# Kernel optimization log

Hardware: AMD Instinct MI355X
Metric: run time of the kernel (lower is better)

## Reference

```python
import jax, jax.numpy as jnp
import numpy as np


def setup_inputs() -> dict:
    key = jax.random.key(0)
    k1, k2 = jax.random.split(key)
    B, H, W, D, K = 32, 32, 32, 256, 8192
    x = jax.random.normal(k1, (B, H, W, D), dtype=jnp.float32)
    # tf.random_uniform_initializer default: U(-0.05, 0.05), shape (embedding_dim, n_embeddings)
    embeddings = jax.random.uniform(k2, (D, K), dtype=jnp.float32, minval=-0.05, maxval=0.05)
    return {"x": x, "embeddings": embeddings}


def reference(x, embeddings):
    beta = 0.25
    D = embeddings.shape[0]
    input_shape = x.shape
    flat = x.reshape(-1, D)  # [N, D]
    similarity = flat @ embeddings  # [N, K]
    distance = (jnp.sum(flat ** 2, axis=1, keepdims=True)
                + jnp.sum(embeddings ** 2, axis=0)
                - 2.0 * similarity)
    idx = jnp.argmin(distance, axis=1)  # [N]
    # one_hot @ embeddings.T is a row gather of embeddings.T
    quantized = jnp.take(embeddings.T, idx, axis=0).reshape(input_shape)
    commitment_loss = jnp.mean((jax.lax.stop_gradient(quantized) - x) ** 2)
    codebook_loss = jnp.mean((quantized - jax.lax.stop_gradient(x)) ** 2)
    loss = beta * commitment_loss + codebook_loss
    # straight-through estimator
    quantized_ste = x + jax.lax.stop_gradient(quantized - x)
    return quantized_ste, loss
```

## Files before the change

kernel.cpp:

```cpp
#include <hip/hip_runtime.h>
#include <hip/hip_bf16.h>
#include <stdint.h>
#include <stddef.h>


typedef float f32x4 __attribute__((ext_vector_type(4)));
typedef _Float16 half8 __attribute__((ext_vector_type(8)));

#define N_ROWS    32768
#define K_CODES   8192
#define TAU       2e-3f
#define TAU2      1.2e-4f
#define CHK       1.5e-3
#define FLAGCAP   8192

#define WS_ETF    0
#define WS_EHT    8388608
#define WS_ELT    12582912
#define WS_ENF    16777216
#define WS_EN64   16809984
#define WS_IDX    16875520
#define WS_SC     17006592
#define WS_CNT    17137664
#define WS_LIST   17137680
#define WS_LIST2  17170448
#define WS_PF1    17203216
#define WS_PF2    17465360
#define WS_PI1    17727504
#define WS_PD     17989648
#define WS_PIR    18513936
#define WS_ROWSUM 18776080
#define WS_FLAGS  18907152
#define WS_NEED   18907168

__device__ __forceinline__ float bf2f(unsigned short u) {
  union { unsigned int i; float f; } v; v.i = ((unsigned int)u) << 16; return v.f;
}
__device__ __forceinline__ float xraw(const void* x, int fx, size_t i) {
  return fx ? ((const float*)x)[i] : bf2f(((const unsigned short*)x)[i]);
}

__global__ void vq_detect(const unsigned short* __restrict__ x,
                          const unsigned short* __restrict__ e,
                          int* __restrict__ flags, int* __restrict__ cnt) {
  __shared__ int fx_s, fe_s;
  const int t = threadIdx.x;
  if (t == 0) { fx_s = 0; fe_s = 0; }
  __syncthreads();
  if (((x[2 * t] >> 7) & 0xFF) >= 0xC0) atomicOr(&fx_s, 1);
  if (((e[2 * t] >> 7) & 0xFF) >= 0xC0) atomicOr(&fe_s, 1);
  __syncthreads();
  if (t == 0) { flags[0] = fx_s; flags[1] = fe_s; cnt[0] = 0; cnt[1] = 0; }
}

__global__ void vq_buildEf(const void* __restrict__ e, const int* __restrict__ flags,
                           float* __restrict__ eTf) {
  __shared__ float tile[64][65];
  const int t = threadIdx.x;
  const int fe = flags[1];
  const int d0 = (blockIdx.x & 3) * 64;
  const int k0 = (blockIdx.x >> 2) * 64;
  const float* ef = (const float*)e;
  const unsigned short* eu = (const unsigned short*)e;
#pragma unroll
  for (int i = 0; i < 16; ++i) {
    const int idx = i * 256 + t;
    const int dd = idx >> 6, kk = idx & 63;
    const size_t src = (size_t)(d0 + dd) * 8192 + (k0 + kk);
    tile[dd][kk] = fe ? ef[src] : bf2f(eu[src]);
  }
  __syncthreads();
#pragma unroll
  for (int i = 0; i < 16; ++i) {
    const int idx = i * 256 + t;
    const int kr = idx >> 6, dc = idx & 63;
    eTf[(size_t)(k0 + kr) * 256 + (d0 + dc)] = tile[dc][kr];
  }
}

__global__ void vq_buildEsplit(const float* __restrict__ eTf, _Float16* __restrict__ eHt,
                               _Float16* __restrict__ eLt,
                               float* __restrict__ enF, double* __restrict__ en64) {
  const int t = threadIdx.x;
  const int r = blockIdx.x * 8 + (t >> 5);
  const int d0 = (t & 31) * 8;
  const float* src = eTf + (size_t)r * 256 + d0;
  double s = 0.0;
  _Float16 h[8], l[8];
#pragma unroll
  for (int j = 0; j < 8; ++j) {
    const float v = src[j];
    h[j] = (_Float16)v;
    l[j] = (_Float16)(v - (float)h[j]);
    s += (double)v * (double)v;
  }
  const size_t o = (size_t)((r >> 4) * 8 + (d0 >> 5)) * 512 + ((d0 >> 3) & 3) * 128 + (r & 15) * 8;
  *(half8*)(eHt + o) = *(const half8*)h;
  *(half8*)(eLt + o) = *(const half8*)l;
#pragma unroll
  for (int off = 1; off <= 16; off <<= 1) s += __shfl_xor(s, off);
  if ((t & 31) == 0) { en64[r] = s; enF[r] = (float)s; }
}

__global__ __launch_bounds__(512, 4) void vq_main(
    const void* __restrict__ x,
    const _Float16* __restrict__ eHt,
    const float* __restrict__ enorm,
    const int* __restrict__ flags,
    int* __restrict__ idxOut, float* __restrict__ scOut,
    int* __restrict__ cnt, int* __restrict__ lst) {
  __shared__ unsigned char smem[65536];
  const int t = threadIdx.x;
  const int wv = t >> 6, lane = t & 63;
  const int i16 = lane & 15, q = lane >> 4;
  const int n0 = blockIdx.x * 64;
  const int fx = flags[0];

  {
    const int row = t >> 3, col = t & 7;
#pragma unroll
    for (int g = 0; g < 4; ++g) {
      float v[8];
      if (fx) {
        const float* xf = (const float*)x;
        *(f32x4*)&v[0] = *(const f32x4*)(xf + (size_t)(n0 + row) * 256 + col * 32 + g * 8);
        *(f32x4*)&v[4] = *(const f32x4*)(xf + (size_t)(n0 + row) * 256 + col * 32 + g * 8 + 4);
      } else {
        const unsigned short* xu = (const unsigned short*)x;
#pragma unroll
        for (int j = 0; j < 8; ++j)
          v[j] = bf2f(xu[(size_t)(n0 + row) * 256 + col * 32 + g * 8 + j]);
      }
      _Float16 h[8], l[8];
#pragma unroll
      for (int j = 0; j < 8; ++j) {
        h[j] = (_Float16)v[j];
        l[j] = (_Float16)(v[j] - (float)h[j]);
      }
      const int off = ((col * 64 + g * 16) ^ ((row & 7) << 4));
      *(half8*)(smem + row * 512 + off) = *(const half8*)h;
      *(half8*)(smem + 32768 + row * 512 + off) = *(const half8*)l;
    }
  }
  __syncthreads();

  f32x4 acc[4][4];
#pragma unroll
  for (int mt = 0; mt < 4; ++mt)
#pragma unroll
    for (int nt = 0; nt < 4; ++nt) acc[mt][nt] = (f32x4){0.f, 0.f, 0.f, 0.f};
  float b1[4], b2[4]; int i1[4];
#pragma unroll
  for (int nt = 0; nt < 4; ++nt) { b1[nt] = 3.4e38f; b2[nt] = 3.4e38f; i1[nt] = 0x7fffffff; }

  const int swz = (i16 & 7) << 4;

  for (int ct = 0; ct < 16; ++ct) {
    const int cb = wv * 1024 + ct * 64;
#pragma unroll 2
    for (int s = 0; s < 8; ++s) {
      half8 A[4];
#pragma unroll
      for (int mt = 0; mt < 4; ++mt)
        A[mt] = *(const half8*)(eHt + (size_t)(cb / 16 + mt) * 4096 + s * 512 + lane * 8);
      const int boff = (s * 64 + q * 16) ^ swz;
      {
        half8 B[4];
#pragma unroll
        for (int nt = 0; nt < 4; ++nt)
          B[nt] = *(const half8*)(smem + (nt * 16 + i16) * 512 + boff);
#pragma unroll
        for (int mt = 0; mt < 4; ++mt)
#pragma unroll
          for (int nt = 0; nt < 4; ++nt)
            acc[mt][nt] = __builtin_amdgcn_mfma_f32_16x16x32_f16(A[mt], B[nt], acc[mt][nt], 0, 0, 0);
      }
      {
        half8 B[4];
#pragma unroll
        for (int nt = 0; nt < 4; ++nt)
          B[nt] = *(const half8*)(smem + 32768 + (nt * 16 + i16) * 512 + boff);
#pragma unroll
        for (int mt = 0; mt < 4; ++mt)
#pragma unroll
          for (int nt = 0; nt < 4; ++nt)
            acc[mt][nt] = __builtin_amdgcn_mfma_f32_16x16x32_f16(A[mt], B[nt], acc[mt][nt], 0, 0, 0);
      }
    }
#pragma unroll
    for (int mt = 0; mt < 4; ++mt) {
      const f32x4 en = *(const f32x4*)(enorm + cb + mt * 16 + q * 4);
#pragma unroll
      for (int nt = 0; nt < 4; ++nt) {
#pragma unroll
        for (int r = 0; r < 4; ++r) {
          const float sc = fmaf(-2.f, acc[mt][nt][r], en[r]);
          const int code = cb + mt * 16 + q * 4 + r;
          b2[nt] = fminf(b2[nt], fmaxf(b1[nt], sc));
          if (sc < b1[nt]) { b1[nt] = sc; i1[nt] = code; }
        }
        acc[mt][nt] = (f32x4){0.f, 0.f, 0.f, 0.f};
      }
    }
  }

#pragma unroll
  for (int off = 16; off <= 32; off <<= 1) {
#pragma unroll
    for (int nt = 0; nt < 4; ++nt) {
      const float os  = __shfl_xor(b1[nt], off);
      const int   oi  = __shfl_xor(i1[nt], off);
      const float os2 = __shfl_xor(b2[nt], off);
      const float nb2 = fminf(fminf(b2[nt], os2), fmaxf(b1[nt], os));
      const bool take = (os < b1[nt]) || (os == b1[nt] && oi < i1[nt]);
      b1[nt] = take ? os : b1[nt];
      i1[nt] = take ? oi : i1[nt];
      b2[nt] = nb2;
    }
  }

  __syncthreads();
  float* redS  = (float*)(smem + 32768);
  int*   redI  = (int*)(smem + 32768 + 2048);
  float* redS2 = (float*)(smem + 32768 + 4096);
  if (q == 0) {
#pragma unroll
    for (int nt = 0; nt < 4; ++nt) {
      const int rr = wv * 64 + nt * 16 + i16;
      redS[rr] = b1[nt]; redI[rr] = i1[nt]; redS2[rr] = b2[nt];
    }
  }
  __syncthreads();
  if (t < 64) {
    float B1 = 3.4e38f, B2 = 3.4e38f; int I1 = 0x7fffffff;
#pragma unroll
    for (int w = 0; w < 8; ++w) {
      const float s1 = redS[w * 64 + t]; const int ii = redI[w * 64 + t]; const float s2 = redS2[w * 64 + t];
      const float nb2 = fminf(fminf(B2, s2), fmaxf(B1, s1));
      const bool take = (s1 < B1) || (s1 == B1 && ii < I1);
      B1 = take ? s1 : B1; I1 = take ? ii : I1; B2 = nb2;
    }
    idxOut[n0 + t] = I1;
    scOut[n0 + t] = B1;
    if (B2 - B1 < TAU) {
      const int p = atomicAdd(cnt, 1);
      if (p < FLAGCAP) lst[p] = n0 + t;
    }
  }
}

__global__ __launch_bounds__(512) void vq_refine(
    const void* __restrict__ x,
    const _Float16* __restrict__ eHt, const _Float16* __restrict__ eLt,
    const float* __restrict__ enorm, const int* __restrict__ flags,
    const int* __restrict__ cnt, const int* __restrict__ lst,
    float* __restrict__ pf1, float* __restrict__ pf2, int* __restrict__ pi1,
    int* __restrict__ cnt1) {
  __shared__ unsigned char smem[65536];
  const int t = threadIdx.x;
  const int wv = t >> 6, lane = t & 63;
  const int i16 = lane & 15, q = lane >> 4;
  const int fx = flags[0];
  const int m = cnt[0];
  if (m > FLAGCAP) {
    if (blockIdx.x == 0 && t == 0) cnt1[0] = N_ROWS;
    return;
  }
  const int units = ((m + 63) >> 6) * 8;
  const int swz = (i16 & 7) << 4;

  for (int u = blockIdx.x; u < units; u += gridDim.x) {
    const int g = u >> 3, sl = u & 7;
    __syncthreads();
    {
      const int row = t >> 3, col = t & 7;
      const int gi = g * 64 + row;
      const int n = (gi < m) ? (lst[gi] & (N_ROWS - 1)) : 0;
#pragma unroll
      for (int gg = 0; gg < 4; ++gg) {
        float v[8];
        if (fx) {
          const float* xf = (const float*)x;
          *(f32x4*)&v[0] = *(const f32x4*)(xf + (size_t)n * 256 + col * 32 + gg * 8);
          *(f32x4*)&v[4] = *(const f32x4*)(xf + (size_t)n * 256 + col * 32 + gg * 8 + 4);
        } else {
          const unsigned short* xu = (const unsigned short*)x;
#pragma unroll
          for (int j = 0; j < 8; ++j)
            v[j] = bf2f(xu[(size_t)n * 256 + col * 32 + gg * 8 + j]);
        }
        _Float16 h[8], l[8];
#pragma unroll
        for (int j = 0; j < 8; ++j) {
          h[j] = (_Float16)v[j];
          l[j] = (_Float16)(v[j] - (float)h[j]);
        }
        const int off = ((col * 64 + gg * 16) ^ ((row & 7) << 4));
        *(half8*)(smem + row * 512 + off) = *(const half8*)h;
        *(half8*)(smem + 32768 + row * 512 + off) = *(const half8*)l;
      }
    }
    __syncthreads();

    f32x4 acc[4][4];
#pragma unroll
    for (int mt = 0; mt < 4; ++mt)
#pragma unroll
      for (int nt = 0; nt < 4; ++nt) acc[mt][nt] = (f32x4){0.f, 0.f, 0.f, 0.f};
    float b1[4], b2[4]; int i1[4];
#pragma unroll
    for (int nt = 0; nt < 4; ++nt) { b1[nt] = 3.4e38f; b2[nt] = 3.4e38f; i1[nt] = 0x7fffffff; }

    for (int ct = 0; ct < 2; ++ct) {
      const int cb = sl * 1024 + wv * 128 + ct * 64;
#pragma unroll
      for (int s = 0; s < 8; ++s) {
        half8 Ah[4], Al[4];
#pragma unroll
        for (int mt = 0; mt < 4; ++mt) {
          const size_t ab = (size_t)(cb / 16 + mt) * 4096 + s * 512 + lane * 8;
          Ah[mt] = *(const half8*)(eHt + ab);
          Al[mt] = *(const half8*)(eLt + ab);
        }
        const int boff = (s * 64 + q * 16) ^ swz;
        {
          half8 B[4];
#pragma unroll
          for (int nt = 0; nt < 4; ++nt)
            B[nt] = *(const half8*)(smem + (nt * 16 + i16) * 512 + boff);
#pragma unroll
          for (int mt = 0; mt < 4; ++mt)
#pragma unroll
            for (int nt = 0; nt < 4; ++nt) {
              acc[mt][nt] = __builtin_amdgcn_mfma_f32_16x16x32_f16(Ah[mt], B[nt], acc[mt][nt], 0, 0, 0);
              acc[mt][nt] = __builtin_amdgcn_mfma_f32_16x16x32_f16(Al[mt], B[nt], acc[mt][nt], 0, 0, 0);
            }
        }
        {
          half8 B[4];
#pragma unroll
          for (int nt = 0; nt < 4; ++nt)
            B[nt] = *(const half8*)(smem + 32768 + (nt * 16 + i16) * 512 + boff);
#pragma unroll
          for (int mt = 0; mt < 4; ++mt)
#pragma unroll
            for (int nt = 0; nt < 4; ++nt)
              acc[mt][nt] = __builtin_amdgcn_mfma_f32_16x16x32_f16(Ah[mt], B[nt], acc[mt][nt], 0, 0, 0);
        }
      }
#pragma unroll
      for (int mt = 0; mt < 4; ++mt) {
        const f32x4 en = *(const f32x4*)(enorm + cb + mt * 16 + q * 4);
#pragma unroll
        for (int nt = 0; nt < 4; ++nt) {
#pragma unroll
          for (int r = 0; r < 4; ++r) {
            const float sc = fmaf(-2.f, acc[mt][nt][r], en[r]);
            const int code = cb + mt * 16 + q * 4 + r;
            b2[nt] = fminf(b2[nt], fmaxf(b1[nt], sc));
            if (sc < b1[nt]) { b1[nt] = sc; i1[nt] = code; }
          }
          acc[mt][nt] = (f32x4){0.f, 0.f, 0.f, 0.f};
        }
      }
    }

#pragma unroll
    for (int off = 16; off <= 32; off <<= 1) {
#pragma unroll
      for (int nt = 0; nt < 4; ++nt) {
        const float os  = __shfl_xor(b1[nt], off);
        const int   oi  = __shfl_xor(i1[nt], off);
        const float os2 = __shfl_xor(b2[nt], off);
        const float nb2 = fminf(fminf(b2[nt], os2), fmaxf(b1[nt], os));
        const bool take = (os < b1[nt]) || (os == b1[nt] && oi < i1[nt]);
        b1[nt] = take ? os : b1[nt];
        i1[nt] = take ? oi : i1[nt];
        b2[nt] = nb2;
      }
    }

    __syncthreads();
    float* redS  = (float*)(smem + 32768);
    int*   redI  = (int*)(smem + 32768 + 2048);
    float* redS2 = (float*)(smem + 32768 + 4096);
    if (q == 0) {
#pragma unroll
      for (int nt = 0; nt < 4; ++nt) {
        const int rr = wv * 64 + nt * 16 + i16;
        redS[rr] = b1[nt]; redI[rr] = i1[nt]; redS2[rr] = b2[nt];
      }
    }
    __syncthreads();
    if (t < 64) {
      float B1 = 3.4e38f, B2 = 3.4e38f; int I1 = 0x7fffffff;
#pragma unroll
      for (int w = 0; w < 8; ++w) {
        const float s1 = redS[w * 64 + t]; const int ii = redI[w * 64 + t]; const float s2 = redS2[w * 64 + t];
        const float nb2 = fminf(fminf(B2, s2), fmaxf(B1, s1));
        const bool take = (s1 < B1) || (s1 == B1 && ii < I1);
        B1 = take ? s1 : B1; I1 = take ? ii : I1; B2 = nb2;
      }
      const int gi = g * 64 + t;
      if (gi < m) { pf1[gi * 8 + sl] = B1; pf2[gi * 8 + sl] = B2; pi1[gi * 8 + sl] = I1; }
    }
  }
}

__global__ void vq_resolveR(const int* __restrict__ cnt, const int* __restrict__ lst,
                            const float* __restrict__ pf1, const float* __restrict__ pf2,
                            const int* __restrict__ pi1,
                            int* __restrict__ idxOut, float* __restrict__ scOut,
                            int* __restrict__ cnt1, int* __restrict__ lst2) {
  const int m = cnt[0];
  if (m > FLAGCAP) return;
  const int li = blockIdx.x * 256 + threadIdx.x;
  if (li >= m) return;
  float B1 = 3.4e38f, B2 = 3.4e38f; int I1 = 0x7fffffff;
#pragma unroll
  for (int sl = 0; sl < 8; ++sl) {
    const float s1 = pf1[li * 8 + sl]; const int ii = pi1[li * 8 + sl]; const float s2 = pf2[li * 8 + sl];
    const float nb2 = fminf(fminf(B2, s2), fmaxf(B1, s1));
    const bool take = (s1 < B1) || (s1 == B1 && ii < I1);
    B1 = take ? s1 : B1; I1 = take ? ii : I1; B2 = nb2;
  }
  const int n = lst[li] & (N_ROWS - 1);
  idxOut[n] = I1;
  scOut[n] = B1;
  if (B2 - B1 < TAU2) {
    const int p = atomicAdd(cnt1, 1);
    if (p < FLAGCAP) lst2[p] = n;
  }
}

__global__ void vq_gathercheck(const void* __restrict__ x, const float* __restrict__ eTf,
                               const int* __restrict__ flags, const int* __restrict__ idx,
                               const float* __restrict__ sc,
                               float* __restrict__ out, float* __restrict__ rowsum,
                               int* __restrict__ cnt1, int* __restrict__ lst2) {
  const int t = threadIdx.x;
  const int gid = blockIdx.x * 256 + t;
  const int n = gid >> 5, s = gid & 31;
  const int fx = flags[0];
  const int code = idx[n] & (K_CODES - 1);
  const f32x4 q0 = *(const f32x4*)(eTf + (size_t)code * 256 + s * 8);
  const f32x4 q1 = *(const f32x4*)(eTf + (size_t)code * 256 + s * 8 + 4);
  *(f32x4*)(out + (size_t)n * 256 + s * 8) = q0;
  *(f32x4*)(out + (size_t)n * 256 + s * 8 + 4) = q1;
  double d2 = 0.0, x2 = 0.0;
#pragma unroll
  for (int j = 0; j < 4; ++j) {
    const double xv0 = (double)xraw(x, fx, (size_t)n * 256 + s * 8 + j);
    const double xv1 = (double)xraw(x, fx, (size_t)n * 256 + s * 8 + 4 + j);
    const double da = (double)q0[j] - xv0;
    const double db = (double)q1[j] - xv1;
    d2 += da * da + db * db;
    x2 += xv0 * xv0 + xv1 * xv1;
  }
#pragma unroll
  for (int off = 16; off >= 1; off >>= 1) {
    d2 += __shfl_xor(d2, off);
    x2 += __shfl_xor(x2, off);
  }
  if (s == 0) {
    rowsum[n] = (float)d2;
    if (fabs(d2 - (x2 + (double)sc[n])) > CHK) {
      const int p = atomicAdd(cnt1, 1);
      if (p < FLAGCAP) lst2[p] = n;
    }
  }
}

__global__ void vq_rescan8(const void* __restrict__ x, const float* __restrict__ eTf,
                           const double* __restrict__ en64, const int* __restrict__ flags,
                           const int* __restrict__ cnt1, const int* __restrict__ lst2,
                           double* __restrict__ pd, int* __restrict__ pir,
                           int* __restrict__ idxOut) {
  __shared__ float sxx[256];
  __shared__ double wS[4]; __shared__ int wI[4];
  const int t = threadIdx.x;
  const int lane = t & 63, wv = t >> 6;
  const int fx = flags[0];
  const int m = cnt1[0];
  if (m <= FLAGCAP) {
    const int units = m * 8;
    for (int u = blockIdx.x; u < units; u += gridDim.x) {
      const int li = u >> 3, sl = u & 7;
      const int n = lst2[li] & (N_ROWS - 1);
      __syncthreads();
      sxx[t] = xraw(x, fx, (size_t)n * 256 + t);
      __syncthreads();
      const f32x4 xv = *(const f32x4*)&sxx[lane * 4];
      double best = 1e300; int bi = 0x7fffffff;
      for (int i = 0; i < 256; ++i) {
        const int c = sl * 1024 + wv * 256 + i;
        const f32x4 ev = *(const f32x4*)(eTf + (size_t)c * 256 + lane * 4);
        double s = (double)ev[0] * (double)xv[0] + (double)ev[1] * (double)xv[1]
                 + (double)ev[2] * (double)xv[2] + (double)ev[3] * (double)xv[3];
#pragma unroll
        for (int off = 32; off >= 1; off >>= 1) s += __shfl_xor(s, off);
        const double dist = en64[c] - 2.0 * s;
        if (dist < best) { best = dist; bi = c; }
      }
      if (lane == 0) { wS[wv] = best; wI[wv] = bi; }
      __syncthreads();
      if (t == 0) {
        double B = wS[0]; int I = wI[0];
#pragma unroll
        for (int w = 1; w < 4; ++w)
          if (wS[w] < B || (wS[w] == B && wI[w] < I)) { B = wS[w]; I = wI[w]; }
        pd[li * 8 + sl] = B; pir[li * 8 + sl] = I;
      }
    }
  } else {
    for (int n = blockIdx.x; n < N_ROWS; n += gridDim.x) {
      __syncthreads();
      sxx[t] = xraw(x, fx, (size_t)n * 256 + t);
      __syncthreads();
      const f32x4 xv = *(const f32x4*)&sxx[lane * 4];
      double best = 1e300; int bi = 0x7fffffff;
      for (int i = 0; i < 2048; ++i) {
        const int c = wv * 2048 + i;
        const f32x4 ev = *(const f32x4*)(eTf + (size_t)c * 256 + lane * 4);
        double s = (double)ev[0] * (double)xv[0] + (double)ev[1] * (double)xv[1]
                 + (double)ev[2] * (double)xv[2] + (double)ev[3] * (double)xv[3];
#pragma unroll
        for (int off = 32; off >= 1; off >>= 1) s += __shfl_xor(s, off);
        const double dist = en64[c] - 2.0 * s;
        if (dist < best) { best = dist; bi = c; }
      }
      if (lane == 0) { wS[wv] = best; wI[wv] = bi; }
      __syncthreads();
      if (t == 0) {
        double B = wS[0]; int I = wI[0];
#pragma unroll
        for (int w = 1; w < 4; ++w)
          if (wS[w] < B || (wS[w] == B && wI[w] < I)) { B = wS[w]; I = wI[w]; }
        idxOut[n] = I;
      }
    }
  }
}

__global__ void vq_resolve(const void* __restrict__ x, const float* __restrict__ eTf,
                           const int* __restrict__ flags,
                           const int* __restrict__ cnt1, const int* __restrict__ lst2,
                           const double* __restrict__ pd, const int* __restrict__ pir,
                           int* __restrict__ idxOut, float* __restrict__ out,
                           float* __restrict__ rowsum) {
  __shared__ double rS[256];
  __shared__ int bcode;
  const int t = threadIdx.x;
  const int fx = flags[0];
  const int m = cnt1[0];
  if (m <= FLAGCAP) {
    for (int li = blockIdx.x; li < m; li += gridDim.x) {
      const int n = lst2[li] & (N_ROWS - 1);
      if (t == 0) {
        double B = pd[li * 8]; int I = pir[li * 8];
#pragma unroll
        for (int sl = 1; sl < 8; ++sl) {
          const double s = pd[li * 8 + sl]; const int ii = pir[li * 8 + sl];
          if (s < B || (s == B && ii < I)) { B = s; I = ii; }
        }
        idxOut[n] = I; bcode = I;
      }
      __syncthreads();
      const float qv = eTf[(size_t)bcode * 256 + t];
      out[(size_t)n * 256 + t] = qv;
      const double dq = (double)qv - (double)xraw(x, fx, (size_t)n * 256 + t);
      rS[t] = dq * dq;
      __syncthreads();
      if (t == 0) {
        double a = 0.0;
        for (int j = 0; j < 256; ++j) a += rS[j];
        rowsum[n] = (float)a;
      }
      __syncthreads();
    }
  } else {
    for (int n = blockIdx.x; n < N_ROWS; n += gridDim.x) {
      const int code = idxOut[n] & (K_CODES - 1);
      const float qv = eTf[(size_t)code * 256 + t];
      out[(size_t)n * 256 + t] = qv;
      const double dq = (double)qv - (double)xraw(x, fx, (size_t)n * 256 + t);
      rS[t] = dq * dq;
      __syncthreads();
      if (t == 0) {
        double a = 0.0;
        for (int j = 0; j < 256; ++j) a += rS[j];
        rowsum[n] = (float)a;
      }
      __syncthreads();
    }
  }
}

__global__ void vq_loss(const float* __restrict__ rowsum, float* __restrict__ lossOut) {
  __shared__ double sd[256];
  const int t = threadIdx.x;
  double a = 0.0;
  for (int i = t; i < N_ROWS; i += 256) a += (double)rowsum[i];
  sd[t] = a;
  __syncthreads();
  if (t == 0) {
    double tot = 0.0;
    for (int j = 0; j < 256; ++j) tot += sd[j];
    lossOut[0] = (float)(1.25 * (tot / 8388608.0));
  }
}

__global__ void vq_marker(const int* __restrict__ flags, float* __restrict__ out) {
  if (threadIdx.x == 0 && flags[0] == 0)
    out[0] = 272.0f + 16.0f * (float)flags[1];
}

extern "C" void kernel_launch(void* const* d_in, const int* in_sizes, int n_in,
                              void* d_out, int out_size, void* d_ws, size_t ws_size,
                              hipStream_t stream) {
  (void)out_size;
  if (ws_size < (size_t)WS_NEED) return;

  const void* x = d_in[0];
  const void* e = d_in[1];
  if (n_in >= 2 && in_sizes[0] == 2097152 && in_sizes[1] == 8388608) {
    x = d_in[1]; e = d_in[0];
  }
  float* out = (float*)d_out;
  char* ws = (char*)d_ws;

  float* eTf     = (float*)(ws + WS_ETF);
  _Float16* eHt  = (_Float16*)(ws + WS_EHT);
  _Float16* eLt  = (_Float16*)(ws + WS_ELT);
  float* enF     = (float*)(ws + WS_ENF);
  double* en64   = (double*)(ws + WS_EN64);
  int* idx       = (int*)(ws + WS_IDX);
  float* sc      = (float*)(ws + WS_SC);
  int* cnt       = (int*)(ws + WS_CNT);
  int* lst       = (int*)(ws + WS_LIST);
  int* lst2      = (int*)(ws + WS_LIST2);
  float* pf1     = (float*)(ws + WS_PF1);
  float* pf2     = (float*)(ws + WS_PF2);
  int* pi1       = (int*)(ws + WS_PI1);
  double* pd     = (double*)(ws + WS_PD);
  int* pir       = (int*)(ws + WS_PIR);
  float* rowsum  = (float*)(ws + WS_ROWSUM);
  int* flags     = (int*)(ws + WS_FLAGS);

  (void)hipGetLastError();
  vq_detect<<<1, 256, 0, stream>>>((const unsigned short*)x, (const unsigned short*)e, flags, cnt);
  vq_buildEf<<<512, 256, 0, stream>>>(e, flags, eTf);
  vq_buildEsplit<<<1024, 256, 0, stream>>>(eTf, eHt, eLt, enF, en64);
  vq_main<<<N_ROWS / 64, 512, 0, stream>>>(x, eHt, enF, flags, idx, sc, cnt, lst);
  vq_refine<<<1024, 512, 0, stream>>>(x, eHt, eLt, enF, flags, cnt, lst, pf1, pf2, pi1, cnt + 1);
  vq_resolveR<<<FLAGCAP / 256, 256, 0, stream>>>(cnt, lst, pf1, pf2, pi1, idx, sc, cnt + 1, lst2);
  vq_gathercheck<<<N_ROWS * 32 / 256, 256, 0, stream>>>(x, eTf, flags, idx, sc, out, rowsum, cnt + 1, lst2);
  vq_rescan8<<<2048, 256, 0, stream>>>(x, eTf, en64, flags, cnt + 1, lst2, pd, pir, idx);
  vq_resolve<<<2048, 256, 0, stream>>>(x, eTf, flags, cnt + 1, lst2, pd, pir, idx, out, rowsum);
  vq_loss<<<1, 256, 0, stream>>>(rowsum, out + 8388608);
  vq_marker<<<1, 64, 0, stream>>>(flags, out);

  if (hipGetLastError() != hipSuccess)
    hipMemsetAsync(d_out, 0x42, 4, stream);
}
```

Baseline: 500.8 us.

## Drop low-half x split in main scan, widen margin, fuse codebook preprocessing

```diff
diff --git a/kernel.cpp b/kernel.cpp
--- a/kernel.cpp
+++ b/kernel.cpp
@@ -9,7 +9,7 @@
 
 #define N_ROWS    32768
 #define K_CODES   8192
-#define TAU       2e-3f
+#define TAU       3e-3f
 #define TAU2      1.2e-4f
 #define CHK       1.5e-3
 #define FLAGCAP   8192
@@ -19,19 +19,20 @@
 #define WS_ELT    12582912
 #define WS_ENF    16777216
 #define WS_EN64   16809984
-#define WS_IDX    16875520
-#define WS_SC     17006592
-#define WS_CNT    17137664
-#define WS_LIST   17137680
-#define WS_LIST2  17170448
-#define WS_PF1    17203216
-#define WS_PF2    17465360
-#define WS_PI1    17727504
-#define WS_PD     17989648
-#define WS_PIR    18513936
-#define WS_ROWSUM 18776080
-#define WS_FLAGS  18907152
-#define WS_NEED   18907168
+#define WS_ENP    16875520
+#define WS_IDX    17137664
+#define WS_SC     17268736
+#define WS_CNT    17399808
+#define WS_LIST   17399824
+#define WS_LIST2  17432592
+#define WS_PF1    17465360
+#define WS_PF2    17727504
+#define WS_PI1    17989648
+#define WS_PD     18251792
+#define WS_PIR    18776080
+#define WS_ROWSUM 19038224
+#define WS_FLAGS  19169296
+#define WS_NEED   19169312
 
 __device__ __forceinline__ float bf2f(unsigned short u) {
   union { unsigned int i; float f; } v; v.i = ((unsigned int)u) << 16; return v.f;
@@ -53,12 +54,14 @@
   if (t == 0) { flags[0] = fx_s; flags[1] = fe_s; cnt[0] = 0; cnt[1] = 0; }
 }
 
-__global__ void vq_buildEf(const void* __restrict__ e, const int* __restrict__ flags,
-                           float* __restrict__ eTf) {
+__global__ void vq_buildAll(const void* __restrict__ e, const int* __restrict__ flags,
+                            float* __restrict__ eTf, _Float16* __restrict__ eHt,
+                            _Float16* __restrict__ eLt, double* __restrict__ enp) {
   __shared__ float tile[64][65];
   const int t = threadIdx.x;
   const int fe = flags[1];
-  const int d0 = (blockIdx.x & 3) * 64;
+  const int dt = blockIdx.x & 3;
+  const int d0 = dt * 64;
   const int k0 = (blockIdx.x >> 2) * 64;
   const float* ef = (const float*)e;
   const unsigned short* eu = (const unsigned short*)e;
@@ -76,30 +79,38 @@
     const int kr = idx >> 6, dc = idx & 63;
     eTf[(size_t)(k0 + kr) * 256 + (d0 + dc)] = tile[dc][kr];
   }
-}
-
-__global__ void vq_buildEsplit(const float* __restrict__ eTf, _Float16* __restrict__ eHt,
-                               _Float16* __restrict__ eLt,
-                               float* __restrict__ enF, double* __restrict__ en64) {
-  const int t = threadIdx.x;
-  const int r = blockIdx.x * 8 + (t >> 5);
-  const int d0 = (t & 31) * 8;
-  const float* src = eTf + (size_t)r * 256 + d0;
-  double s = 0.0;
-  _Float16 h[8], l[8];
-#pragma unroll
-  for (int j = 0; j < 8; ++j) {
-    const float v = src[j];
-    h[j] = (_Float16)v;
-    l[j] = (_Float16)(v - (float)h[j]);
-    s += (double)v * (double)v;
-  }
-  const size_t o = (size_t)((r >> 4) * 8 + (d0 >> 5)) * 512 + ((d0 >> 3) & 3) * 128 + (r & 15) * 8;
-  *(half8*)(eHt + o) = *(const half8*)h;
-  *(half8*)(eLt + o) = *(const half8*)l;
-#pragma unroll
-  for (int off = 1; off <= 16; off <<= 1) s += __shfl_xor(s, off);
-  if ((t & 31) == 0) { en64[r] = s; enF[r] = (float)s; }
+#pragma unroll
+  for (int i = 0; i < 2; ++i) {
+    const int u = i * 256 + t;
+    const int kr = u >> 3, g = u & 7;
+    const int k = k0 + kr, d = d0 + g * 8;
+    _Float16 h[8], l[8];
+    double s = 0.0;
+#pragma unroll
+    for (int j = 0; j < 8; ++j) {
+      const float v = tile[g * 8 + j][kr];
+      h[j] = (_Float16)v;
+      l[j] = (_Float16)(v - (float)h[j]);
+      s += (double)v * (double)v;
+    }
+    const size_t o = (size_t)((k >> 4) * 8 + (d >> 5)) * 512 + ((d >> 3) & 3) * 128 + (k & 15) * 8;
+    *(half8*)(eHt + o) = *(const half8*)h;
+    *(half8*)(eLt + o) = *(const half8*)l;
+#pragma unroll
+    for (int off = 1; off <= 4; off <<= 1) s += __shfl_xor(s, off);
+    if ((t & 7) == 0) enp[(size_t)dt * 8192 + k] = s;
+  }
+}
+
+__global__ void vq_finNorm(const double* __restrict__ enp, double* __restrict__ en64,
+                           float* __restrict__ enF) {
+  const int k = blockIdx.x * 256 + threadIdx.x;
+  double s = enp[k];
+  s += enp[8192 + k];
+  s += enp[16384 + k];
+  s += enp[24576 + k];
+  en64[k] = s;
+  enF[k] = (float)s;
 }
 
 __global__ __launch_bounds__(512, 4) void vq_main(
@@ -109,7 +120,7 @@
     const int* __restrict__ flags,
     int* __restrict__ idxOut, float* __restrict__ scOut,
     int* __restrict__ cnt, int* __restrict__ lst) {
-  __shared__ unsigned char smem[65536];
+  __shared__ unsigned char smem[38912];
   const int t = threadIdx.x;
   const int wv = t >> 6, lane = t & 63;
   const int i16 = lane & 15, q = lane >> 4;
@@ -131,15 +142,11 @@
         for (int j = 0; j < 8; ++j)
           v[j] = bf2f(xu[(size_t)(n0 + row) * 256 + col * 32 + g * 8 + j]);
       }
-      _Float16 h[8], l[8];
-#pragma unroll
-      for (int j = 0; j < 8; ++j) {
-        h[j] = (_Float16)v[j];
-        l[j] = (_Float16)(v[j] - (float)h[j]);
-      }
+      _Float16 h[8];
+#pragma unroll
+      for (int j = 0; j < 8; ++j) h[j] = (_Float16)v[j];
       const int off = ((col * 64 + g * 16) ^ ((row & 7) << 4));
       *(half8*)(smem + row * 512 + off) = *(const half8*)h;
-      *(half8*)(smem + 32768 + row * 512 + off) = *(const half8*)l;
     }
   }
   __syncthreads();
@@ -163,29 +170,16 @@
 #pragma unroll
       for (int mt = 0; mt < 4; ++mt)
         A[mt] = *(const half8*)(eHt + (size_t)(cb / 16 + mt) * 4096 + s * 512 + lane * 8);
+      half8 B[4];
       const int boff = (s * 64 + q * 16) ^ swz;
-      {
-        half8 B[4];
+#pragma unroll
+      for (int nt = 0; nt < 4; ++nt)
+        B[nt] = *(const half8*)(smem + (nt * 16 + i16) * 512 + boff);
+#pragma unroll
+      for (int mt = 0; mt < 4; ++mt)
 #pragma unroll
         for (int nt = 0; nt < 4; ++nt)
-          B[nt] = *(const half8*)(smem + (nt * 16 + i16) * 512 + boff);
-#pragma unroll
-        for (int mt = 0; mt < 4; ++mt)
-#pragma unroll
-          for (int nt = 0; nt < 4; ++nt)
-            acc[mt][nt] = __builtin_amdgcn_mfma_f32_16x16x32_f16(A[mt], B[nt], acc[mt][nt], 0, 0, 0);
-      }
-      {
-        half8 B[4];
-#pragma unroll
-        for (int nt = 0; nt < 4; ++nt)
-          B[nt] = *(const half8*)(smem + 32768 + (nt * 16 + i16) * 512 + boff);
-#pragma unroll
-        for (int mt = 0; mt < 4; ++mt)
-#pragma unroll
-          for (int nt = 0; nt < 4; ++nt)
-            acc[mt][nt] = __builtin_amdgcn_mfma_f32_16x16x32_f16(A[mt], B[nt], acc[mt][nt], 0, 0, 0);
-      }
+          acc[mt][nt] = __builtin_amdgcn_mfma_f32_16x16x32_f16(A[mt], B[nt], acc[mt][nt], 0, 0, 0);
     }
 #pragma unroll
     for (int mt = 0; mt < 4; ++mt) {
@@ -195,9 +189,10 @@
 #pragma unroll
         for (int r = 0; r < 4; ++r) {
           const float sc = fmaf(-2.f, acc[mt][nt][r], en[r]);
-          const int code = cb + mt * 16 + q * 4 + r;
-          b2[nt] = fminf(b2[nt], fmaxf(b1[nt], sc));
-          if (sc < b1[nt]) { b1[nt] = sc; i1[nt] = code; }
+          b2[nt] = __builtin_amdgcn_fmed3f(sc, b1[nt], b2[nt]);
+          const bool better = sc < b1[nt];
+          b1[nt] = better ? sc : b1[nt];
+          i1[nt] = better ? (cb + mt * 16 + q * 4 + r) : i1[nt];
         }
         acc[mt][nt] = (f32x4){0.f, 0.f, 0.f, 0.f};
       }
@@ -356,9 +351,10 @@
 #pragma unroll
           for (int r = 0; r < 4; ++r) {
             const float sc = fmaf(-2.f, acc[mt][nt][r], en[r]);
-            const int code = cb + mt * 16 + q * 4 + r;
-            b2[nt] = fminf(b2[nt], fmaxf(b1[nt], sc));
-            if (sc < b1[nt]) { b1[nt] = sc; i1[nt] = code; }
+            b2[nt] = __builtin_amdgcn_fmed3f(sc, b1[nt], b2[nt]);
+            const bool better = sc < b1[nt];
+            b1[nt] = better ? sc : b1[nt];
+            i1[nt] = better ? (cb + mt * 16 + q * 4 + r) : i1[nt];
           }
           acc[mt][nt] = (f32x4){0.f, 0.f, 0.f, 0.f};
         }
@@ -634,6 +630,7 @@
   _Float16* eLt  = (_Float16*)(ws + WS_ELT);
   float* enF     = (float*)(ws + WS_ENF);
   double* en64   = (double*)(ws + WS_EN64);
+  double* enp    = (double*)(ws + WS_ENP);
   int* idx       = (int*)(ws + WS_IDX);
   float* sc      = (float*)(ws + WS_SC);
   int* cnt       = (int*)(ws + WS_CNT);
@@ -649,8 +646,8 @@
 
   (void)hipGetLastError();
   vq_detect<<<1, 256, 0, stream>>>((const unsigned short*)x, (const unsigned short*)e, flags, cnt);
-  vq_buildEf<<<512, 256, 0, stream>>>(e, flags, eTf);
-  vq_buildEsplit<<<1024, 256, 0, stream>>>(eTf, eHt, eLt, enF, en64);
+  vq_buildAll<<<512, 256, 0, stream>>>(e, flags, eTf, eHt, eLt, enp);
+  vq_finNorm<<<32, 256, 0, stream>>>(enp, en64, enF);
   vq_main<<<N_ROWS / 64, 512, 0, stream>>>(x, eHt, enF, flags, idx, sc, cnt, lst);
   vq_refine<<<1024, 512, 0, stream>>>(x, eHt, eLt, enF, flags, cnt, lst, pf1, pf2, pi1, cnt + 1);
   vq_resolveR<<<FLAGCAP / 256, 256, 0, stream>>>(cnt, lst, pf1, pf2, pi1, idx, sc, cnt + 1, lst2);
```

New measurement: 423.5 us. -15.4%, faster.
